# Optimization experiments

Measured on AMD Instinct MI355X. Metric: run time of the kernel, lower is better.

Reference implementation:

```python
import jax, jax.numpy as jnp
import numpy as np

B, P, D, V = 8192, 32, 128, 100000  # batch, max path len, embed dim, label_num


def setup_inputs() -> dict:
    key = jax.random.key(0)
    k1, k2, k3, k4, k5, k6 = jax.random.split(key, 6)
    return {
        "hidden_": jax.random.normal(k1, (B, D), dtype=jnp.float32),
        "target": jax.random.randint(k2, (B,), 0, V, dtype=jnp.int64),
        "target_path": jax.random.randint(k3, (B, P), 0, V, dtype=jnp.int64),
        "target_path_len": jax.random.randint(k4, (B,), 1, P, dtype=jnp.int64),
        "target_code": jax.random.randint(k5, (B, P), 0, 2, dtype=jnp.int64),
        "embed_table": jax.random.normal(k6, (V, D), dtype=jnp.float32) * 0.02,
    }


def reference(hidden_, target, target_path, target_path_len, target_code, embed_table):
    # embeds: [B, P, D] gather of tree-node vectors along each label's path
    embeds = embed_table[target_path]
    # per-node score: sigmoid(<node_vec, hidden>) -> [B, P]
    score = jax.nn.sigmoid(jnp.einsum("bpd,bd->bp", embeds, hidden_))
    flag = target_code.astype(jnp.float32)
    # BCE-style per-node loss, exactly as the TF code writes it
    loss = -jnp.log(flag * score + (1.0 - flag) * (1.0 - score))
    # ragged path mask: positions < target_path_len are valid (tf.ragged.range + batch_gather)
    mask = (jnp.arange(P)[None, :] < target_path_len[:, None]).astype(jnp.float32)
    # reduce_mean over the ragged tensor = sum of valid losses / total valid count
    return jnp.sum(loss * mask) / jnp.sum(mask)
```

## Files before the change

kernel.cpp:

```cpp
#include <hip/hip_runtime.h>

#define BB 8192
#define PP 32
#define DD 128

__global__ __launch_bounds__(256) void hs_loss_kernel(
    const float* __restrict__ hidden,
    const int*   __restrict__ path,
    const int*   __restrict__ path_len,
    const int*   __restrict__ code,
    const float* __restrict__ embed,
    float2* __restrict__ partials)
{
    const int tid = threadIdx.x;
    const int w   = tid >> 6;
    const int l   = tid & 63;
    const int q   = l >> 4;
    const int ql  = l & 15;
    const int lp  = l & 31;
    const int b   = blockIdx.x * 4 + w;

    __shared__ float plds[4][PP * 17];
    float* const myp = plds[w];

    const int len   = path_len[b];
    const int idx_l = path[b * PP + lp];
    const int cd_l  = code[b * PP + lp];

    const float4 h0 = ((const float4*)hidden)[b * (DD / 4) + ql];
    const float4 h1 = ((const float4*)hidden)[b * (DD / 4) + 16 + ql];

    float4 e0[8], e1[8];
    #pragma unroll
    for (int j = 0; j < 8; ++j) {
        const int pid = q * 8 + j;
        const int idx = __shfl(idx_l, pid);
        if (pid < len) {
            const float4* erow = (const float4*)(embed + (size_t)idx * DD);
            e0[j] = erow[ql];
            e1[j] = erow[16 + ql];
        }
    }

    #pragma unroll
    for (int j = 0; j < 8; ++j) {
        const int pid = q * 8 + j;
        if (pid < len) {
            const float p8 =
                e0[j].x * h0.x + e0[j].y * h0.y + e0[j].z * h0.z + e0[j].w * h0.w +
                e1[j].x * h1.x + e1[j].y * h1.y + e1[j].z * h1.z + e1[j].w * h1.w;
            myp[pid * 17 + ql] = p8;
        }
    }

    const int kbase = (l >> 5) * 8;
    float psum = 0.0f;
    #pragma unroll
    for (int k = 0; k < 8; ++k) psum += myp[lp * 17 + kbase + k];
    const float dot = psum + __shfl_xor(psum, 32);

    float loss = 0.0f;
    if (l < 32 && lp < len) {
        const float z = cd_l ? -dot : dot;
        loss = fmaxf(z, 0.0f) + __logf(1.0f + __expf(-fabsf(z)));
    }
    #pragma unroll
    for (int m = 1; m <= 32; m <<= 1) loss += __shfl_xor(loss, m);
    if (l == 0) partials[b] = make_float2(loss, (float)len);
}

__global__ __launch_bounds__(1024) void hs_finalize_kernel(
    const float2* __restrict__ partials, float* __restrict__ out)
{
    const int tid = threadIdx.x;
    float ls = 0.0f, cs = 0.0f;
    #pragma unroll
    for (int k = 0; k < BB / 1024; ++k) {
        const float2 v = partials[tid + k * 1024];
        ls += v.x;
        cs += v.y;
    }
    #pragma unroll
    for (int m = 1; m <= 32; m <<= 1) {
        ls += __shfl_xor(ls, m);
        cs += __shfl_xor(cs, m);
    }
    __shared__ float s_l[16], s_c[16];
    const int wave = tid >> 6;
    if ((tid & 63) == 0) { s_l[wave] = ls; s_c[wave] = cs; }
    __syncthreads();
    if (tid == 0) {
        float L = 0.0f, C = 0.0f;
        #pragma unroll
        for (int wv = 0; wv < 16; ++wv) { L += s_l[wv]; C += s_c[wv]; }
        out[0] = L / C;
    }
}

extern "C" void kernel_launch(void* const* d_in, const int* in_sizes, int n_in,
                              void* d_out, int out_size, void* d_ws, size_t ws_size,
                              hipStream_t stream) {
    const float* hidden   = (const float*)d_in[0];
    const int*   path     = (const int*)d_in[2];
    const int*   path_len = (const int*)d_in[3];
    const int*   code     = (const int*)d_in[4];
    const float* embed    = (const float*)d_in[5];
    float*  out      = (float*)d_out;
    float2* partials = (float2*)d_ws;

    hs_loss_kernel<<<BB / 4, 256, 0, stream>>>(hidden, path, path_len, code,
                                               embed, partials);
    hs_finalize_kernel<<<1, 1024, 0, stream>>>(partials, out);
}
```

Measured before the change: 100.5 us.

## Load each embedding row with a half-wave of 32 lanes and batch by length

Each embedding row is now read by 32 lanes with one float4 per lane, so a full 512-byte row comes in as one contiguous access and each wave covers two rows at a time. The old split, where each lane held two float4s spaced 256 bytes apart, is gone. Loads are issued in batches of 8 path positions and a whole batch is skipped once it passes the path length, which cuts loads in flight for short paths. The cost is more LDS partial storage (33 floats per position), a longer 16-term reduction, and less memory-level parallelism per wave than the old 16 outstanding loads.

```diff
diff --git a/kernel.cpp b/kernel.cpp
--- a/kernel.cpp
+++ b/kernel.cpp
@@ -15,48 +15,48 @@
     const int tid = threadIdx.x;
     const int w   = tid >> 6;
     const int l   = tid & 63;
-    const int q   = l >> 4;
-    const int ql  = l & 15;
-    const int lp  = l & 31;
+    const int h   = l >> 5;
+    const int hl  = l & 31;
     const int b   = blockIdx.x * 4 + w;
 
-    __shared__ float plds[4][PP * 17];
+    __shared__ float plds[4][PP * 33];
     float* const myp = plds[w];
 
     const int len   = path_len[b];
-    const int idx_l = path[b * PP + lp];
-    const int cd_l  = code[b * PP + lp];
+    const int idx_l = path[b * PP + hl];
+    const int cd_l  = code[b * PP + hl];
 
-    const float4 h0 = ((const float4*)hidden)[b * (DD / 4) + ql];
-    const float4 h1 = ((const float4*)hidden)[b * (DD / 4) + 16 + ql];
+    const float4 hv = ((const float4*)(hidden + (size_t)b * DD))[hl];
 
-    float4 e0[8], e1[8];
     #pragma unroll
-    for (int j = 0; j < 8; ++j) {
-        const int pid = q * 8 + j;
-        const int idx = __shfl(idx_l, pid);
-        if (pid < len) {
-            const float4* erow = (const float4*)(embed + (size_t)idx * DD);
-            e0[j] = erow[ql];
-            e1[j] = erow[16 + ql];
+    for (int batch = 0; batch < 4; ++batch) {
+        const int p0 = batch * 8;
+        if (p0 < len) {
+            int pid[4];
+            float4 e[4];
+            #pragma unroll
+            for (int j = 0; j < 4; ++j) {
+                pid[j] = p0 + 2 * j + h;
+                const int idx = __shfl(idx_l, pid[j]);
+                if (pid[j] < len)
+                    e[j] = ((const float4*)(embed + (size_t)idx * DD))[hl];
+            }
+            #pragma unroll
+            for (int j = 0; j < 4; ++j) {
+                if (pid[j] < len) {
+                    const float pr = e[j].x * hv.x + e[j].y * hv.y
+                                   + e[j].z * hv.z + e[j].w * hv.w;
+                    myp[pid[j] * 33 + hl] = pr;
+                }
+            }
         }
     }
 
-    #pragma unroll
-    for (int j = 0; j < 8; ++j) {
-        const int pid = q * 8 + j;
-        if (pid < len) {
-            const float p8 =
-                e0[j].x * h0.x + e0[j].y * h0.y + e0[j].z * h0.z + e0[j].w * h0.w +
-                e1[j].x * h1.x + e1[j].y * h1.y + e1[j].z * h1.z + e1[j].w * h1.w;
-            myp[pid * 17 + ql] = p8;
-        }
-    }
-
-    const int kbase = (l >> 5) * 8;
+    const int lp = l & 31;
+    const int kb = h * 16;
     float psum = 0.0f;
     #pragma unroll
-    for (int k = 0; k < 8; ++k) psum += myp[lp * 17 + kbase + k];
+    for (int k = 0; k < 16; ++k) psum += myp[lp * 33 + kb + k];
     const float dot = psum + __shfl_xor(psum, 32);
 
     float loss = 0.0f;
```

Measured after the change: 100.1 us. No clear change (-0.3%).
